# Kernel optimization log

Measured on AMD Instinct MI355X. Metric: run time of the kernel, lower is better.

The kernel has to match this reference:

```python
import jax, jax.numpy as jnp
import numpy as np

TEMPERATURE = 0.07
MASK_VAL = -65504.0  # torch code's fill value (fp16 min), note: applied BEFORE temperature division
EPS = 1e-8


def setup_inputs() -> dict:
    key = jax.random.key(0)
    z = jax.random.normal(key, (8192, 1024), dtype=jnp.float32)
    return {"z": z}


def reference(z):
    N = z.shape[0]
    # cosine similarity via normalized GEMM (torch clamps norm at eps)
    norms = jnp.maximum(jnp.linalg.norm(z, axis=-1, keepdims=True), EPS)
    zn = z / norms
    cos_sim = zn @ zn.T  # [N, N]
    eye = jnp.eye(N, dtype=bool)
    cos_sim = jnp.where(eye, MASK_VAL, cos_sim) / TEMPERATURE
    # pos_mask = eye rolled by N//2 along dim 0 -> pos_mask[i, (i - N//2) % N] = True
    idx = jnp.arange(N)
    pos = cos_sim[idx, (idx - N // 2) % N]
    nll = -pos + jax.nn.logsumexp(cos_sim, axis=-1)
    return nll.mean()
```

## Files before the change

kernel.cpp:

```cpp
#include <hip/hip_runtime.h>
#include <hip/hip_bf16.h>


#define N 8192
#define D 1024
#define INV_T 14.285714285714286f

typedef __bf16 bf16x8 __attribute__((ext_vector_type(8)));
typedef float f32x4 __attribute__((ext_vector_type(4)));

__device__ inline void gload16(const void* g, void* l) {
  __builtin_amdgcn_global_load_lds(
      (const __attribute__((address_space(1))) void*)g,
      (__attribute__((address_space(3))) void*)l, 16, 0, 0);
}

__device__ inline unsigned short f32_to_bf16(float f) {
  unsigned int u = __float_as_uint(f);
  unsigned int r = (u + 0x7FFFu + ((u >> 16) & 1u)) >> 16;
  return (unsigned short)r;
}

__global__ __launch_bounds__(256) void k_normalize(const float* __restrict__ z,
                                                   unsigned short* __restrict__ zn,
                                                   float* __restrict__ rowsum) {
  const int row = blockIdx.x;
  const int t = threadIdx.x;
  if (row < 32) rowsum[row * 256 + t] = 0.0f;
  const float4 v = ((const float4*)(z + (size_t)row * D))[t];
  float ss = v.x * v.x + v.y * v.y + v.z * v.z + v.w * v.w;
#pragma unroll
  for (int off = 32; off > 0; off >>= 1) ss += __shfl_down(ss, off, 64);
  __shared__ float red[4];
  __shared__ float s_inv;
  if ((t & 63) == 0) red[t >> 6] = ss;
  __syncthreads();
  if (t == 0) {
    float tot = red[0] + red[1] + red[2] + red[3];
    s_inv = 1.0f / fmaxf(sqrtf(tot), 1e-8f);
  }
  __syncthreads();
  const float inv = s_inv;
  ushort4 o;
  o.x = f32_to_bf16(v.x * inv);
  o.y = f32_to_bf16(v.y * inv);
  o.z = f32_to_bf16(v.z * inv);
  o.w = f32_to_bf16(v.w * inv);
  ((ushort4*)(zn + (size_t)row * D))[t] = o;
}

__global__ __launch_bounds__(512, 2) void k_tile(const unsigned short* __restrict__ zn,
                                                 float* __restrict__ rowsum,
                                                 float* __restrict__ pos) {
  extern __shared__ __align__(16) char smem[];
  const int tid = threadIdx.x;
  const int w = tid >> 6, l = tid & 63;

  const int b = blockIdx.x;
  int tr = (int)((sqrtf(8.0f * (float)b + 1.0f) - 1.0f) * 0.5f);
  if (tr * (tr + 1) / 2 > b) --tr;
  if ((tr + 1) * (tr + 2) / 2 <= b) ++tr;
  const int tc = b - tr * (tr + 1) / 2;
  const bool diag = (tr == tc);

  const int wr = w >> 1, wc = w & 1;
  const int m = l & 15, kg = l >> 4;
  const int rowA0 = tr * 256, colB0 = tc * 256;

  f32x4 acc[4][8] = {};

  int srow[4], scol[4];
#pragma unroll
  for (int j = 0; j < 4; ++j) {
    int s = j * 512 + tid;
    int r = s >> 3;
    srow[j] = r;
    scol[j] = (s & 7) ^ (r & 7);
  }

  {
    char* ab = smem;
    char* bb = smem + 32768;
#pragma unroll
    for (int j = 0; j < 4; ++j) {
      const int s = j * 512 + tid;
      gload16((const char*)zn + ((size_t)(rowA0 + srow[j]) * 2048 + scol[j] * 16), ab + s * 16);
    }
    if (!diag) {
#pragma unroll
      for (int j = 0; j < 4; ++j) {
        const int s = j * 512 + tid;
        gload16((const char*)zn + ((size_t)(colB0 + srow[j]) * 2048 + scol[j] * 16), bb + s * 16);
      }
    }
  }
  __syncthreads();

  for (int kt = 0; kt < 16; ++kt) {
    if (kt < 15) {
      const size_t kb = (size_t)(kt + 1) * 128;
      char* ab = smem + ((kt + 1) & 1) * 65536;
#pragma unroll
      for (int j = 0; j < 4; ++j) {
        const int s = j * 512 + tid;
        gload16((const char*)zn + ((size_t)(rowA0 + srow[j]) * 2048 + kb + scol[j] * 16), ab + s * 16);
      }
      if (!diag) {
        char* bb = ab + 32768;
#pragma unroll
        for (int j = 0; j < 4; ++j) {
          const int s = j * 512 + tid;
          gload16((const char*)zn + ((size_t)(colB0 + srow[j]) * 2048 + kb + scol[j] * 16), bb + s * 16);
        }
      }
    }
    const char* ab = smem + (kt & 1) * 65536;
    const char* bb = diag ? ab : (ab + 32768);
#pragma unroll
    for (int ks = 0; ks < 2; ++ks) {
      bf16x8 af[4], bfr[8];
      const int csw = ((ks * 4 + kg) ^ (m & 7)) * 16;
#pragma unroll
      for (int mt = 0; mt < 4; ++mt)
        af[mt] = *(const bf16x8*)(ab + (wr * 64 + mt * 16 + m) * 128 + csw);
#pragma unroll
      for (int nt = 0; nt < 8; ++nt)
        bfr[nt] = *(const bf16x8*)(bb + (wc * 128 + nt * 16 + m) * 128 + csw);
#pragma unroll
      for (int mt = 0; mt < 4; ++mt)
#pragma unroll
        for (int nt = 0; nt < 8; ++nt)
          acc[mt][nt] = __builtin_amdgcn_mfma_f32_16x16x32_bf16(af[mt], bfr[nt], acc[mt][nt], 0, 0, 0);
    }
    __syncthreads();
  }

  const int quad = l >> 4;
  const int col = l & 15;
  float cs[8] = {0.f, 0.f, 0.f, 0.f, 0.f, 0.f, 0.f, 0.f};
#pragma unroll
  for (int mt = 0; mt < 4; ++mt) {
    float rs[4] = {0.f, 0.f, 0.f, 0.f};
#pragma unroll
    for (int nt = 0; nt < 8; ++nt) {
      const int gcol = colB0 + wc * 128 + nt * 16 + col;
#pragma unroll
      for (int r = 0; r < 4; ++r) {
        const int grow = rowA0 + wr * 64 + mt * 16 + quad * 4 + r;
        const float t = acc[mt][nt][r] * INV_T;
        if (gcol == (grow ^ (N / 2))) {
          pos[grow] = t;
          pos[gcol] = t;
        }
        const float e = (gcol == grow) ? 0.0f : __expf(t - INV_T);
        rs[r] += e;
        cs[nt] += e;
      }
    }
#pragma unroll
    for (int off = 1; off < 16; off <<= 1) {
#pragma unroll
      for (int r = 0; r < 4; ++r) rs[r] += __shfl_xor(rs[r], off, 64);
    }
    if (col == 0) {
#pragma unroll
      for (int r = 0; r < 4; ++r)
        atomicAdd(&rowsum[rowA0 + wr * 64 + mt * 16 + quad * 4 + r], rs[r]);
    }
  }
  if (!diag) {
#pragma unroll
    for (int nt = 0; nt < 8; ++nt) {
      cs[nt] += __shfl_xor(cs[nt], 16, 64);
      cs[nt] += __shfl_xor(cs[nt], 32, 64);
    }
    if (l < 16) {
#pragma unroll
      for (int nt = 0; nt < 8; ++nt)
        atomicAdd(&rowsum[colB0 + wc * 128 + nt * 16 + l], cs[nt]);
    }
  }
}

__global__ __launch_bounds__(256) void k_final(const float* __restrict__ rowsum,
                                               const float* __restrict__ pos,
                                               float* __restrict__ out) {
  const int t = threadIdx.x;
  float s = 0.f;
  for (int i = t; i < N; i += 256) s += INV_T + __logf(rowsum[i]) - pos[i];
#pragma unroll
  for (int off = 32; off > 0; off >>= 1) s += __shfl_down(s, off, 64);
  __shared__ float red[4];
  if ((t & 63) == 0) red[t >> 6] = s;
  __syncthreads();
  if (t == 0) out[0] = (red[0] + red[1] + red[2] + red[3]) * (1.0f / N);
}

extern "C" void kernel_launch(void* const* d_in, const int* in_sizes, int n_in,
                              void* d_out, int out_size, void* d_ws, size_t ws_size,
                              hipStream_t stream) {
  const float* z = (const float*)d_in[0];
  float* out = (float*)d_out;
  char* ws = (char*)d_ws;
  unsigned short* zn = (unsigned short*)ws;
  float* rowsum = (float*)(ws + (size_t)N * D * 2);
  float* pos = (float*)(ws + (size_t)N * D * 2 + (size_t)N * 4);

  static bool attr_set = false;
  if (!attr_set) {
    hipFuncSetAttribute((const void*)k_tile,
                        hipFuncAttributeMaxDynamicSharedMemorySize, 131072);
    attr_set = true;
  }

  k_normalize<<<N, 256, 0, stream>>>(z, zn, rowsum);
  const int ntiles = (N / 256) * (N / 256 + 1) / 2;
  k_tile<<<ntiles, 512, 131072, stream>>>(zn, rowsum, pos);
  k_final<<<1, 256, 0, stream>>>(rowsum, pos, out);
}
```

Before: 164.0 us.

## Switch similarity GEMM to FP8 MFMA and fuse final reduction via last-block counter

Normalized rows are now quantized to FP8 (scaled by 32) instead of bf16, which halves the bytes loaded per tile and uses the fp8 MFMA path, with accumulators rescaled by INV_T/1024. The K loop is restructured to 8 iterations of 128-byte chunks with 8-byte fragment loads. The separate final kernel is removed: each tile block increments an atomic counter and the last block computes the log-sum-exp mean, saving one launch. FP8 quantization lowers the precision of the cosine similarities, which after scaling by 1/T may push the loss past tolerance.

```diff
diff --git a/kernel.cpp b/kernel.cpp
--- a/kernel.cpp
+++ b/kernel.cpp
@@ -5,8 +5,9 @@
 #define N 8192
 #define D 1024
 #define INV_T 14.285714285714286f
-
-typedef __bf16 bf16x8 __attribute__((ext_vector_type(8)));
+#define NTILES 528
+#define ACC_SCALE (INV_T / 1024.0f)
+
 typedef float f32x4 __attribute__((ext_vector_type(4)));
 
 __device__ inline void gload16(const void* g, void* l) {
@@ -15,18 +16,14 @@
       (__attribute__((address_space(3))) void*)l, 16, 0, 0);
 }
 
-__device__ inline unsigned short f32_to_bf16(float f) {
-  unsigned int u = __float_as_uint(f);
-  unsigned int r = (u + 0x7FFFu + ((u >> 16) & 1u)) >> 16;
-  return (unsigned short)r;
-}
-
 __global__ __launch_bounds__(256) void k_normalize(const float* __restrict__ z,
-                                                   unsigned short* __restrict__ zn,
-                                                   float* __restrict__ rowsum) {
+                                                   unsigned char* __restrict__ zn8,
+                                                   float* __restrict__ rowsum,
+                                                   int* __restrict__ counter) {
   const int row = blockIdx.x;
   const int t = threadIdx.x;
   if (row < 32) rowsum[row * 256 + t] = 0.0f;
+  if (row == 32 && t == 0) *counter = 0;
   const float4 v = ((const float4*)(z + (size_t)row * D))[t];
   float ss = v.x * v.x + v.y * v.y + v.z * v.z + v.w * v.w;
 #pragma unroll
@@ -40,18 +37,17 @@
     s_inv = 1.0f / fmaxf(sqrtf(tot), 1e-8f);
   }
   __syncthreads();
-  const float inv = s_inv;
-  ushort4 o;
-  o.x = f32_to_bf16(v.x * inv);
-  o.y = f32_to_bf16(v.y * inv);
-  o.z = f32_to_bf16(v.z * inv);
-  o.w = f32_to_bf16(v.w * inv);
-  ((ushort4*)(zn + (size_t)row * D))[t] = o;
-}
-
-__global__ __launch_bounds__(512, 2) void k_tile(const unsigned short* __restrict__ zn,
+  const float sc = s_inv * 32.0f;
+  int p = __builtin_amdgcn_cvt_pk_fp8_f32(v.x * sc, v.y * sc, 0, false);
+  p = __builtin_amdgcn_cvt_pk_fp8_f32(v.z * sc, v.w * sc, p, true);
+  ((int*)(zn8 + (size_t)row * D))[t] = p;
+}
+
+__global__ __launch_bounds__(512, 2) void k_tile(const unsigned char* __restrict__ zn8,
                                                  float* __restrict__ rowsum,
-                                                 float* __restrict__ pos) {
+                                                 float* __restrict__ pos,
+                                                 int* __restrict__ counter,
+                                                 float* __restrict__ out) {
   extern __shared__ __align__(16) char smem[];
   const int tid = threadIdx.x;
   const int w = tid >> 6, l = tid & 63;
@@ -84,53 +80,53 @@
 #pragma unroll
     for (int j = 0; j < 4; ++j) {
       const int s = j * 512 + tid;
-      gload16((const char*)zn + ((size_t)(rowA0 + srow[j]) * 2048 + scol[j] * 16), ab + s * 16);
+      gload16((const char*)zn8 + ((size_t)(rowA0 + srow[j]) * D + scol[j] * 16), ab + s * 16);
     }
     if (!diag) {
 #pragma unroll
       for (int j = 0; j < 4; ++j) {
         const int s = j * 512 + tid;
-        gload16((const char*)zn + ((size_t)(colB0 + srow[j]) * 2048 + scol[j] * 16), bb + s * 16);
-      }
-    }
-  }
-  __syncthreads();
-
-  for (int kt = 0; kt < 16; ++kt) {
-    if (kt < 15) {
+        gload16((const char*)zn8 + ((size_t)(colB0 + srow[j]) * D + scol[j] * 16), bb + s * 16);
+      }
+    }
+  }
+  __syncthreads();
+
+  for (int kt = 0; kt < 8; ++kt) {
+    if (kt < 7) {
       const size_t kb = (size_t)(kt + 1) * 128;
       char* ab = smem + ((kt + 1) & 1) * 65536;
 #pragma unroll
       for (int j = 0; j < 4; ++j) {
         const int s = j * 512 + tid;
-        gload16((const char*)zn + ((size_t)(rowA0 + srow[j]) * 2048 + kb + scol[j] * 16), ab + s * 16);
+        gload16((const char*)zn8 + ((size_t)(rowA0 + srow[j]) * D + kb + scol[j] * 16), ab + s * 16);
       }
       if (!diag) {
         char* bb = ab + 32768;
 #pragma unroll
         for (int j = 0; j < 4; ++j) {
           const int s = j * 512 + tid;
-          gload16((const char*)zn + ((size_t)(colB0 + srow[j]) * 2048 + kb + scol[j] * 16), bb + s * 16);
+          gload16((const char*)zn8 + ((size_t)(colB0 + srow[j]) * D + kb + scol[j] * 16), bb + s * 16);
         }
       }
     }
     const char* ab = smem + (kt & 1) * 65536;
     const char* bb = diag ? ab : (ab + 32768);
 #pragma unroll
-    for (int ks = 0; ks < 2; ++ks) {
-      bf16x8 af[4], bfr[8];
-      const int csw = ((ks * 4 + kg) ^ (m & 7)) * 16;
+    for (int ks = 0; ks < 4; ++ks) {
+      long af[4], bfr[8];
+      const int csw = ((2 * ks + (kg >> 1)) ^ (m & 7)) * 16 + (kg & 1) * 8;
 #pragma unroll
       for (int mt = 0; mt < 4; ++mt)
-        af[mt] = *(const bf16x8*)(ab + (wr * 64 + mt * 16 + m) * 128 + csw);
+        af[mt] = *(const long*)(ab + (wr * 64 + mt * 16 + m) * 128 + csw);
 #pragma unroll
       for (int nt = 0; nt < 8; ++nt)
-        bfr[nt] = *(const bf16x8*)(bb + (wc * 128 + nt * 16 + m) * 128 + csw);
+        bfr[nt] = *(const long*)(bb + (wc * 128 + nt * 16 + m) * 128 + csw);
 #pragma unroll
       for (int mt = 0; mt < 4; ++mt)
 #pragma unroll
         for (int nt = 0; nt < 8; ++nt)
-          acc[mt][nt] = __builtin_amdgcn_mfma_f32_16x16x32_bf16(af[mt], bfr[nt], acc[mt][nt], 0, 0, 0);
+          acc[mt][nt] = __builtin_amdgcn_mfma_f32_16x16x32_fp8_fp8(af[mt], bfr[nt], acc[mt][nt], 0, 0, 0);
     }
     __syncthreads();
   }
@@ -147,10 +143,10 @@
 #pragma unroll
       for (int r = 0; r < 4; ++r) {
         const int grow = rowA0 + wr * 64 + mt * 16 + quad * 4 + r;
-        const float t = acc[mt][nt][r] * INV_T;
+        const float t = acc[mt][nt][r] * ACC_SCALE;
         if (gcol == (grow ^ (N / 2))) {
-          pos[grow] = t;
-          pos[gcol] = t;
+          __hip_atomic_store(&pos[grow], t, __ATOMIC_RELAXED, __HIP_MEMORY_SCOPE_AGENT);
+          __hip_atomic_store(&pos[gcol], t, __ATOMIC_RELAXED, __HIP_MEMORY_SCOPE_AGENT);
         }
         const float e = (gcol == grow) ? 0.0f : __expf(t - INV_T);
         rs[r] += e;
@@ -180,20 +176,34 @@
         atomicAdd(&rowsum[colB0 + wc * 128 + nt * 16 + l], cs[nt]);
     }
   }
-}
-
-__global__ __launch_bounds__(256) void k_final(const float* __restrict__ rowsum,
-                                               const float* __restrict__ pos,
-                                               float* __restrict__ out) {
-  const int t = threadIdx.x;
-  float s = 0.f;
-  for (int i = t; i < N; i += 256) s += INV_T + __logf(rowsum[i]) - pos[i];
-#pragma unroll
-  for (int off = 32; off > 0; off >>= 1) s += __shfl_down(s, off, 64);
-  __shared__ float red[4];
-  if ((t & 63) == 0) red[t >> 6] = s;
-  __syncthreads();
-  if (t == 0) out[0] = (red[0] + red[1] + red[2] + red[3]) * (1.0f / N);
+
+  __shared__ int s_last;
+  __syncthreads();
+  __threadfence();
+  if (tid == 0) {
+    int old = __hip_atomic_fetch_add(counter, 1, __ATOMIC_ACQ_REL, __HIP_MEMORY_SCOPE_AGENT);
+    s_last = (old == NTILES - 1);
+  }
+  __syncthreads();
+  if (s_last) {
+    float s = 0.f;
+    for (int i = tid; i < N; i += 512) {
+      const float rsv = __hip_atomic_load(&rowsum[i], __ATOMIC_RELAXED, __HIP_MEMORY_SCOPE_AGENT);
+      const float pv = __hip_atomic_load(&pos[i], __ATOMIC_RELAXED, __HIP_MEMORY_SCOPE_AGENT);
+      s += INV_T + __logf(rsv) - pv;
+    }
+#pragma unroll
+    for (int off = 32; off > 0; off >>= 1) s += __shfl_down(s, off, 64);
+    float* red = (float*)smem;
+    if (l == 0) red[w] = s;
+    __syncthreads();
+    if (tid == 0) {
+      float tot = 0.f;
+#pragma unroll
+      for (int j = 0; j < 8; ++j) tot += red[j];
+      out[0] = tot * (1.0f / N);
+    }
+  }
 }
 
 extern "C" void kernel_launch(void* const* d_in, const int* in_sizes, int n_in,
@@ -202,9 +212,10 @@
   const float* z = (const float*)d_in[0];
   float* out = (float*)d_out;
   char* ws = (char*)d_ws;
-  unsigned short* zn = (unsigned short*)ws;
-  float* rowsum = (float*)(ws + (size_t)N * D * 2);
-  float* pos = (float*)(ws + (size_t)N * D * 2 + (size_t)N * 4);
+  unsigned char* zn8 = (unsigned char*)ws;
+  float* rowsum = (float*)(ws + (size_t)N * D);
+  float* pos = (float*)(ws + (size_t)N * D + (size_t)N * 4);
+  int* counter = (int*)(ws + (size_t)N * D + (size_t)N * 8);
 
   static bool attr_set = false;
   if (!attr_set) {
@@ -213,8 +224,6 @@
     attr_set = true;
   }
 
-  k_normalize<<<N, 256, 0, stream>>>(z, zn, rowsum);
-  const int ntiles = (N / 256) * (N / 256 + 1) / 2;
-  k_tile<<<ntiles, 512, 131072, stream>>>(zn, rowsum, pos);
-  k_final<<<1, 256, 0, stream>>>(rowsum, pos, out);
-}
+  k_normalize<<<N, 256, 0, stream>>>(z, zn8, rowsum, counter);
+  k_tile<<<NTILES, 512, 131072, stream>>>(zn8, rowsum, pos, counter, out);
+}
```

Measured after the change: 221.9 us. 1.35x slower.
